# Kernel optimization log

Hardware: AMD Instinct MI355X
Metric: run time of the kernel (lower is better)

Reference implementation:

```python
import jax, jax.numpy as jnp
import numpy as np

B, S, D_MODEL, N_HEADS, MAX_LEN = 2, 1024, 1024, 16, 1024
D_K = D_MODEL // N_HEADS


def setup_inputs() -> dict:
    key = jax.random.key(0)
    ks = jax.random.split(key, 8)
    w_std = 1.0 / np.sqrt(D_MODEL)  # ~ torch Linear default scale
    inp = {
        "query": jax.random.normal(ks[0], (B, S, D_MODEL), jnp.float32),
        "key": jax.random.normal(ks[1], (B, S, D_MODEL), jnp.float32),
        "value": jax.random.normal(ks[2], (B, S, D_MODEL), jnp.float32),
        "Wq": jax.random.normal(ks[3], (D_MODEL, D_MODEL), jnp.float32) * w_std,
        "Wk": jax.random.normal(ks[4], (D_MODEL, D_MODEL), jnp.float32) * w_std,
        "Wv": jax.random.normal(ks[5], (D_MODEL, D_MODEL), jnp.float32) * w_std,
        "Wo": jax.random.normal(ks[6], (D_MODEL, D_MODEL), jnp.float32) * w_std,
        "bq": jnp.zeros((D_MODEL,), jnp.float32),
        "bk": jnp.zeros((D_MODEL,), jnp.float32),
        "bv": jnp.zeros((D_MODEL,), jnp.float32),
        "bo": jnp.zeros((D_MODEL,), jnp.float32),
        "Er": jax.random.normal(ks[7], (2 * MAX_LEN - 1, D_K), jnp.float32) * 0.02,
    }
    return inp


def _rel_positions(q_len, k_len, max_len):
    pos = jnp.arange(q_len)[:, None] - jnp.arange(k_len)[None, :]
    pos = jnp.clip(pos, -max_len + 1, max_len - 1)
    return pos + max_len - 1  # [q_len, k_len] indices into Er


def reference(query, key, value, Wq, Wk, Wv, Wo, bq, bk, bv, bo, Er):
    b, q_len, d_model = query.shape
    k_len = key.shape[1]
    d_k = Er.shape[-1]
    h = d_model // d_k
    scale = 1.0 / np.sqrt(d_k)

    def proj(x, W, bias):  # torch Linear: x @ W.T + b, then split heads -> [b,h,s,d_k]
        y = x @ W.T + bias
        return y.reshape(b, -1, h, d_k).transpose(0, 2, 1, 3)

    q = proj(query, Wq, bq)
    k = proj(key, Wk, bk)
    v = proj(value, Wv, bv)

    positions = _rel_positions(q_len, k_len, MAX_LEN)  # [q,k]
    # QEr[b,h,q,k] = sum_d q[b,h,q,d] * Er[positions[q,k], d]
    # computed as a full contraction against Er then a gather on the relative axis
    qe_all = jnp.einsum('bhqd,rd->bhqr', q, Er)  # [b,h,q,2*max_len-1]
    qer = jnp.take_along_axis(qe_all, positions[None, None, :, :], axis=-1)  # [b,h,q,k]

    qk = jnp.einsum('bhqd,bhkd->bhqk', q, k)
    scores = (qk + qer) * scale
    p_attn = jax.nn.softmax(scores, axis=-1)  # dropout=0.0 (eval)
    out = jnp.einsum('bhqk,bhkd->bhqd', p_attn, v)

    out = out.transpose(0, 2, 1, 3).reshape(b, q_len, h * d_k)
    return out @ Wo.T + bo
```

## Files before the change

kernel.cpp:

```cpp
#include <hip/hip_runtime.h>
#include <hip/hip_bf16.h>
#include <cstdint>
#include <cstddef>

typedef __attribute__((ext_vector_type(8))) short bf16x8;
typedef __attribute__((ext_vector_type(4))) float f32x4;
typedef unsigned short u16;
typedef unsigned int u32;

#define DEV static __device__ __forceinline__

constexpr int Sc = 1024, DMc = 1024, Hc = 16, DKc = 64;

DEV u16 f2bf(float f) {
  u32 u = __float_as_uint(f);
  return (u16)((u + 0x7FFFu + ((u >> 16) & 1u)) >> 16);
}
DEV float bf2f(u16 h) { return __uint_as_float(((u32)h) << 16); }

DEV void lds_fence() {
  asm volatile("s_waitcnt lgkmcnt(0)" ::: "memory");
  __builtin_amdgcn_sched_barrier(0);
}

#define GLDS16(g, l)                                                        \
  __builtin_amdgcn_global_load_lds(                                         \
      (const __attribute__((address_space(1))) void*)(g),                   \
      (__attribute__((address_space(3))) void*)(l), 16, 0, 0)

struct CvtJob { const float* in; u16* out; int nchunk; int rsh; };
struct CvtArgs { CvtJob j[8]; };

__global__ __launch_bounds__(256) void cvt_kernel(CvtArgs a) {
  CvtJob job = a.j[blockIdx.y];
  int ci = (int)(blockIdx.x * 256 + threadIdx.x);
  if (ci >= job.nchunk) return;
  const float* src = job.in + (size_t)ci * 8;
  float4 v0 = *(const float4*)src;
  float4 v1 = *(const float4*)(src + 4);
  bf16x8 o;
  o[0] = (short)f2bf(v0.x); o[1] = (short)f2bf(v0.y);
  o[2] = (short)f2bf(v0.z); o[3] = (short)f2bf(v0.w);
  o[4] = (short)f2bf(v1.x); o[5] = (short)f2bf(v1.y);
  o[6] = (short)f2bf(v1.z); o[7] = (short)f2bf(v1.w);
  int row = ci >> job.rsh;
  int co = (ci & ~7) | ((ci & 7) ^ (row & 7));
  *(bf16x8*)(job.out + (size_t)co * 8) = o;
}

struct GemmJob { const u16* A; const u16* W; const float* bias; void* out; };
struct GemmArgs { GemmJob p[3]; };

template<int BM, int MODE>
__global__ __launch_bounds__(256, 2) void gemm_bt(GemmArgs G) {
  constexpr int MI = BM / 32;
  __shared__ __align__(16) u16 sA[2][BM * 64];
  __shared__ __align__(16) u16 sB[2][128 * 64];
  const int tid = threadIdx.x, lane = tid & 63, w = tid >> 6;
  const int cl = lane & 15, rg = lane >> 4;
  const int srow = lane >> 3, schk = lane & 7;
  int z, m0, n0;
  if (MODE == 0) {
    int id = blockIdx.x;
    if (id < 256) { z = id >> 7; int r = id & 127; m0 = (r >> 3) * 128; n0 = (r & 7) * 128; }
    else          { z = 2;       int r = id - 256; m0 = (r >> 4) * 128; n0 = (r & 15) * 128; }
  } else {
    z = 0; int id = blockIdx.x; m0 = (id >> 3) * 64; n0 = (id & 7) * 128;
  }
  GemmJob P = G.p[z];
  constexpr int K = 1024;
  const int wm = (w >> 1) * (MI * 16), wn = (w & 1) * 64;
  f32x4 acc[MI][4] = {};

  auto stage = [&](int kt, int b) {
    const u16* Ab = P.A + (size_t)m0 * K + kt * 64;
    const u16* Wb = P.W + (size_t)n0 * K + kt * 64;
    #pragma unroll
    for (int i = 0; i < BM / 32; ++i)
      GLDS16(Ab + (size_t)(i * 32 + w * 8 + srow) * K + schk * 8, &sA[b][(i * 32 + w * 8) * 64]);
    #pragma unroll
    for (int i = 0; i < 4; ++i)
      GLDS16(Wb + (size_t)(i * 32 + w * 8 + srow) * K + schk * 8, &sB[b][(i * 32 + w * 8) * 64]);
  };

  stage(0, 0);
  for (int kt = 0; kt < 16; ++kt) {
    __syncthreads();
    if (kt < 15) stage(kt + 1, (kt + 1) & 1);
    const u16* A_ = sA[kt & 1];
    const u16* B_ = sB[kt & 1];
    #pragma unroll
    for (int kk = 0; kk < 2; ++kk) {
      bf16x8 af[MI], bfr[4];
      #pragma unroll
      for (int mi = 0; mi < MI; ++mi) {
        int row = wm + mi * 16 + cl;
        af[mi] = *(const bf16x8*)(A_ + row * 64 + ((kk * 4 + rg) ^ (row & 7)) * 8);
      }
      #pragma unroll
      for (int ni = 0; ni < 4; ++ni) {
        int row = wn + ni * 16 + cl;
        bfr[ni] = *(const bf16x8*)(B_ + row * 64 + ((kk * 4 + rg) ^ (row & 7)) * 8);
      }
      #pragma unroll
      for (int mi = 0; mi < MI; ++mi)
        #pragma unroll
        for (int ni = 0; ni < 4; ++ni)
          acc[mi][ni] = __builtin_amdgcn_mfma_f32_16x16x32_bf16(af[mi], bfr[ni], acc[mi][ni], 0, 0, 0);
    }
  }
  #pragma unroll
  for (int mi = 0; mi < MI; ++mi) {
    #pragma unroll
    for (int ni = 0; ni < 4; ++ni) {
      #pragma unroll
      for (int j = 0; j < 4; ++j) {
        int m = m0 + wm + mi * 16 + rg * 4 + j;
        int n = n0 + wn + ni * 16 + cl;
        if (MODE == 1) {
          ((float*)P.out)[(size_t)m * DMc + n] = acc[mi][ni][j] + P.bias[n];
        } else if (z < 2) {
          float v = acc[mi][ni][j] + P.bias[n];
          int h = n >> 6, d = n & 63;
          int c2 = (d >> 3) ^ (m & 7);
          ((u16*)P.out)[((size_t)((m >> 10) * Hc + h) * Sc + (m & 1023)) * DKc + c2 * 8 + (d & 7)] = f2bf(v);
        } else {
          float v = acc[mi][ni][j] + P.bias[m];
          int d = m & 63, h = m >> 6, bb = n >> 10, s = n & 1023;
          int c2 = ((s & 63) >> 3) ^ (d & 7);
          ((u16*)P.out)[((size_t)(bb * Hc + h) * DKc + d) * Sc + (s & ~63) + c2 * 8 + (s & 7)] = f2bf(v);
        }
      }
    }
  }
}

__global__ __launch_bounds__(256, 2) void attn_rel(
    const u16* __restrict__ qg, const u16* __restrict__ kg,
    const u16* __restrict__ vtg, const u16* __restrict__ erg,
    u16* __restrict__ og) {
  __shared__ __align__(16) u16 sK[2][64 * 64];
  __shared__ __align__(16) u16 sV[2][64 * 64];
  __shared__ __align__(16) u16 sT[4][16 * 80];
  __shared__ __align__(16) u16 sP[4][16 * 72];
  const int tid = threadIdx.x, lane = tid & 63, w = tid >> 6;
  const int cl = lane & 15, rg = lane >> 4;
  const int key = cl & 7;
  const int bh = blockIdx.x & 31, qt = blockIdx.x >> 5, q0 = qt * 64;

  const u16* qrow = qg + ((size_t)bh * Sc + q0 + w * 16 + cl) * DKc;
  bf16x8 qf0 = *(const bf16x8*)(qrow + (rg ^ key) * 8);
  bf16x8 qf1 = *(const bf16x8*)(qrow + ((rg + 4) ^ key) * 8);
  f32x4 oacc[4] = {};
  float lrow[4] = {0.f, 0.f, 0.f, 0.f};
  u16* Tw = sT[w];
  u16* Pw = sP[w];
  const u16* kbase = kg + (size_t)bh * Sc * DKc;
  const u16* vbase = vtg + (size_t)bh * DKc * Sc;

  auto stage = [&](int t, int b) {
    const u16* ks = kbase + t * 64 * 64;
    #pragma unroll
    for (int i = 0; i < 2; ++i) {
      GLDS16(ks + (i * 32 + w * 8) * 64 + lane * 8, &sK[b][(i * 32 + w * 8) * 64]);
      GLDS16(vbase + (size_t)(i * 32 + w * 8 + (lane >> 3)) * Sc + t * 64 + (lane & 7) * 8,
             &sV[b][(i * 32 + w * 8) * 64]);
    }
  };

  stage(0, 0);
  for (int t = 0; t < 16; ++t) {
    __syncthreads();
    if (t < 15) stage(t + 1, (t + 1) & 1);
    const u16* Kb = sK[t & 1];
    const u16* Vb = sV[t & 1];
    const u16* ebase = erg + (size_t)(q0 - t * 64 + 960) * DKc;

    f32x4 sc4[4];
    #pragma unroll
    for (int nc = 0; nc < 4; ++nc) {
      const u16* kr = Kb + (nc * 16 + cl) * 64;
      bf16x8 b0 = *(const bf16x8*)(kr + (rg ^ key) * 8);
      bf16x8 b1 = *(const bf16x8*)(kr + ((rg + 4) ^ key) * 8);
      f32x4 a = {};
      a = __builtin_amdgcn_mfma_f32_16x16x32_bf16(qf0, b0, a, 0, 0, 0);
      a = __builtin_amdgcn_mfma_f32_16x16x32_bf16(qf1, b1, a, 0, 0, 0);
      sc4[nc] = a;
    }
    #pragma unroll
    for (int rc0 = 0; rc0 < 5; ++rc0) {
      const u16* er = ebase + (size_t)((w + rc0) * 16 + cl) * DKc;
      bf16x8 b0 = *(const bf16x8*)(er + (rg ^ key) * 8);
      bf16x8 b1 = *(const bf16x8*)(er + ((rg + 4) ^ key) * 8);
      f32x4 a = {};
      a = __builtin_amdgcn_mfma_f32_16x16x32_bf16(qf0, b0, a, 0, 0, 0);
      a = __builtin_amdgcn_mfma_f32_16x16x32_bf16(qf1, b1, a, 0, 0, 0);
      #pragma unroll
      for (int j = 0; j < 4; ++j)
        Tw[(rg * 4 + j) * 80 + rc0 * 16 + cl] = f2bf(a[j]);
    }
    lds_fence();
    #pragma unroll
    for (int j = 0; j < 4; ++j) {
      const int qi = rg * 4 + j;
      #pragma unroll
      for (int nc = 0; nc < 4; ++nc) {
        int rl = qi + 63 - (nc * 16 + cl);
        float p = __expf((sc4[nc][j] + bf2f(Tw[qi * 80 + rl])) * 0.125f);
        lrow[j] += p;
        Pw[qi * 72 + nc * 16 + cl] = f2bf(p);
      }
    }
    lds_fence();
    bf16x8 pa0 = *(const bf16x8*)(Pw + cl * 72 + rg * 8);
    bf16x8 pa1 = *(const bf16x8*)(Pw + cl * 72 + 32 + rg * 8);
    #pragma unroll
    for (int dc = 0; dc < 4; ++dc) {
      const u16* vr = Vb + (dc * 16 + cl) * 64;
      bf16x8 b0 = *(const bf16x8*)(vr + (rg ^ key) * 8);
      bf16x8 b1 = *(const bf16x8*)(vr + ((rg + 4) ^ key) * 8);
      oacc[dc] = __builtin_amdgcn_mfma_f32_16x16x32_bf16(pa0, b0, oacc[dc], 0, 0, 0);
      oacc[dc] = __builtin_amdgcn_mfma_f32_16x16x32_bf16(pa1, b1, oacc[dc], 0, 0, 0);
    }
  }
  #pragma unroll
  for (int j = 0; j < 4; ++j) {
    float l = lrow[j];
    #pragma unroll
    for (int off = 1; off < 16; off <<= 1) l += __shfl_xor(l, off);
    lrow[j] = l;
  }
  const int b_ = bh >> 4, h = bh & 15;
  #pragma unroll
  for (int dc = 0; dc < 4; ++dc) {
    #pragma unroll
    for (int j = 0; j < 4; ++j) {
      int qr = q0 + w * 16 + rg * 4 + j;
      float v = oacc[dc][j] / lrow[j];
      int col = dc * 16 + cl;
      int c2 = (col >> 3) ^ (qr & 7);
      og[((size_t)(b_ * Sc + qr)) * DMc + h * 64 + c2 * 8 + (col & 7)] = f2bf(v);
    }
  }
}

extern "C" void kernel_launch(void* const* d_in, const int* in_sizes, int n_in,
                              void* d_out, int out_size, void* d_ws, size_t ws_size,
                              hipStream_t stream) {
  (void)in_sizes; (void)n_in; (void)out_size; (void)ws_size;
  const float* query = (const float*)d_in[0];
  const float* key_  = (const float*)d_in[1];
  const float* value = (const float*)d_in[2];
  const float* Wq = (const float*)d_in[3];
  const float* Wk = (const float*)d_in[4];
  const float* Wv = (const float*)d_in[5];
  const float* Wo = (const float*)d_in[6];
  const float* bq = (const float*)d_in[7];
  const float* bk = (const float*)d_in[8];
  const float* bv = (const float*)d_in[9];
  const float* bo = (const float*)d_in[10];
  const float* Er = (const float*)d_in[11];

  char* p = (char*)d_ws;
  size_t off = 0;
  auto alloc = [&](size_t bytes) {
    char* r = p + off;
    off += (bytes + 255) & ~(size_t)255;
    return r;
  };
  u16* Xq  = (u16*)alloc((size_t)2048 * 1024 * 2);
  u16* Xk  = (u16*)alloc((size_t)2048 * 1024 * 2);
  u16* Xv  = (u16*)alloc((size_t)2048 * 1024 * 2);
  u16* Wqb = (u16*)alloc((size_t)1024 * 1024 * 2);
  u16* Wkb = (u16*)alloc((size_t)1024 * 1024 * 2);
  u16* Wvb = (u16*)alloc((size_t)1024 * 1024 * 2);
  u16* Wob = (u16*)alloc((size_t)1024 * 1024 * 2);
  u16* Erb = (u16*)alloc((size_t)2048 * 64 * 2);
  u16* qh  = (u16*)alloc((size_t)2048 * 1024 * 2);
  u16* kh  = (u16*)alloc((size_t)2048 * 1024 * 2);
  u16* vt  = (u16*)alloc((size_t)2048 * 1024 * 2);
  u16* attnb = (u16*)alloc((size_t)2048 * 1024 * 2);

  CvtArgs ca;
  ca.j[0] = {query, Xq, 262144, 7};
  ca.j[1] = {key_,  Xk, 262144, 7};
  ca.j[2] = {value, Xv, 262144, 7};
  ca.j[3] = {Wq, Wqb, 131072, 7};
  ca.j[4] = {Wk, Wkb, 131072, 7};
  ca.j[5] = {Wv, Wvb, 131072, 7};
  ca.j[6] = {Wo, Wob, 131072, 7};
  ca.j[7] = {Er, Erb, 16376, 3};
  cvt_kernel<<<dim3(1024, 8, 1), 256, 0, stream>>>(ca);
  hipMemsetAsync(Erb + (size_t)2047 * 64, 0, 64 * sizeof(u16), stream);

  GemmArgs gp;
  gp.p[0] = {Xq, Wqb, bq, (void*)qh};
  gp.p[1] = {Xk, Wkb, bk, (void*)kh};
  gp.p[2] = {Wvb, Xv, bv, (void*)vt};
  gemm_bt<128, 0><<<dim3(384, 1, 1), 256, 0, stream>>>(gp);

  attn_rel<<<dim3(512, 1, 1), 256, 0, stream>>>(qh, kh, vt, Erb, attnb);

  GemmArgs go;
  go.p[0] = {attnb, Wob, bo, d_out};
  go.p[1] = go.p[0];
  go.p[2] = go.p[0];
  gemm_bt<64, 1><<<dim3(256, 1, 1), 256, 0, stream>>>(go);
}
```

Before: 106.2 us.

## Split attention over key halves with a merge kernel and pad LDS rows

Splits each attention block's 16 key tiles into two halves, so 1024 blocks are launched instead of 512, and writes unnormalized fp32 partial outputs and row sums to a workspace. A new merge kernel adds the two partials, normalizes them and writes the bf16 swizzled attention output. This is valid because the softmax uses no max subtraction. It also raises the occupancy hint to 3, pads the LDS row strides (80 to 84, 72 to 76) to reduce bank conflicts, and folds the Er padding memset into the convert kernel. The trade-off is extra fp32 traffic for the partials and one more kernel launch, in exchange for better CU fill on 256 CUs.

```diff
diff --git a/kernel.cpp b/kernel.cpp
--- a/kernel.cpp
+++ b/kernel.cpp
@@ -28,21 +28,23 @@
       (const __attribute__((address_space(1))) void*)(g),                   \
       (__attribute__((address_space(3))) void*)(l), 16, 0, 0)
 
-struct CvtJob { const float* in; u16* out; int nchunk; int rsh; };
+struct CvtJob { const float* in; u16* out; int nchunk; int rsh; int nreal; };
 struct CvtArgs { CvtJob j[8]; };
 
 __global__ __launch_bounds__(256) void cvt_kernel(CvtArgs a) {
   CvtJob job = a.j[blockIdx.y];
   int ci = (int)(blockIdx.x * 256 + threadIdx.x);
   if (ci >= job.nchunk) return;
-  const float* src = job.in + (size_t)ci * 8;
-  float4 v0 = *(const float4*)src;
-  float4 v1 = *(const float4*)(src + 4);
-  bf16x8 o;
-  o[0] = (short)f2bf(v0.x); o[1] = (short)f2bf(v0.y);
-  o[2] = (short)f2bf(v0.z); o[3] = (short)f2bf(v0.w);
-  o[4] = (short)f2bf(v1.x); o[5] = (short)f2bf(v1.y);
-  o[6] = (short)f2bf(v1.z); o[7] = (short)f2bf(v1.w);
+  bf16x8 o = {};
+  if (ci < job.nreal) {
+    const float* src = job.in + (size_t)ci * 8;
+    float4 v0 = *(const float4*)src;
+    float4 v1 = *(const float4*)(src + 4);
+    o[0] = (short)f2bf(v0.x); o[1] = (short)f2bf(v0.y);
+    o[2] = (short)f2bf(v0.z); o[3] = (short)f2bf(v0.w);
+    o[4] = (short)f2bf(v1.x); o[5] = (short)f2bf(v1.y);
+    o[6] = (short)f2bf(v1.z); o[7] = (short)f2bf(v1.w);
+  }
   int row = ci >> job.rsh;
   int co = (ci & ~7) | ((ci & 7) ^ (row & 7));
   *(bf16x8*)(job.out + (size_t)co * 8) = o;
@@ -135,18 +137,20 @@
   }
 }
 
-__global__ __launch_bounds__(256, 2) void attn_rel(
+__global__ __launch_bounds__(256, 3) void attn_rel(
     const u16* __restrict__ qg, const u16* __restrict__ kg,
     const u16* __restrict__ vtg, const u16* __restrict__ erg,
-    u16* __restrict__ og) {
+    float* __restrict__ Opart, float* __restrict__ lpart) {
   __shared__ __align__(16) u16 sK[2][64 * 64];
   __shared__ __align__(16) u16 sV[2][64 * 64];
-  __shared__ __align__(16) u16 sT[4][16 * 80];
-  __shared__ __align__(16) u16 sP[4][16 * 72];
+  __shared__ __align__(16) u16 sT[4][16 * 84];
+  __shared__ __align__(16) u16 sP[4][16 * 76];
   const int tid = threadIdx.x, lane = tid & 63, w = tid >> 6;
   const int cl = lane & 15, rg = lane >> 4;
   const int key = cl & 7;
-  const int bh = blockIdx.x & 31, qt = blockIdx.x >> 5, q0 = qt * 64;
+  const int bh = blockIdx.x & 31, qt = (blockIdx.x >> 5) & 15, half = blockIdx.x >> 9;
+  const int q0 = qt * 64;
+  const int t0 = half * 8;
 
   const u16* qrow = qg + ((size_t)bh * Sc + q0 + w * 16 + cl) * DKc;
   bf16x8 qf0 = *(const bf16x8*)(qrow + (rg ^ key) * 8);
@@ -168,12 +172,13 @@
     }
   };
 
-  stage(0, 0);
-  for (int t = 0; t < 16; ++t) {
+  stage(t0, 0);
+  for (int tt = 0; tt < 8; ++tt) {
+    const int t = t0 + tt;
     __syncthreads();
-    if (t < 15) stage(t + 1, (t + 1) & 1);
-    const u16* Kb = sK[t & 1];
-    const u16* Vb = sV[t & 1];
+    if (tt < 7) stage(t + 1, (tt + 1) & 1);
+    const u16* Kb = sK[tt & 1];
+    const u16* Vb = sV[tt & 1];
     const u16* ebase = erg + (size_t)(q0 - t * 64 + 960) * DKc;
 
     f32x4 sc4[4];
@@ -197,7 +202,7 @@
       a = __builtin_amdgcn_mfma_f32_16x16x32_bf16(qf1, b1, a, 0, 0, 0);
       #pragma unroll
       for (int j = 0; j < 4; ++j)
-        Tw[(rg * 4 + j) * 80 + rc0 * 16 + cl] = f2bf(a[j]);
+        Tw[(rg * 4 + j) * 84 + rc0 * 16 + cl] = f2bf(a[j]);
     }
     lds_fence();
     #pragma unroll
@@ -206,14 +211,14 @@
       #pragma unroll
       for (int nc = 0; nc < 4; ++nc) {
         int rl = qi + 63 - (nc * 16 + cl);
-        float p = __expf((sc4[nc][j] + bf2f(Tw[qi * 80 + rl])) * 0.125f);
+        float p = __expf((sc4[nc][j] + bf2f(Tw[qi * 84 + rl])) * 0.125f);
         lrow[j] += p;
-        Pw[qi * 72 + nc * 16 + cl] = f2bf(p);
+        Pw[qi * 76 + nc * 16 + cl] = f2bf(p);
       }
     }
     lds_fence();
-    bf16x8 pa0 = *(const bf16x8*)(Pw + cl * 72 + rg * 8);
-    bf16x8 pa1 = *(const bf16x8*)(Pw + cl * 72 + 32 + rg * 8);
+    bf16x8 pa0 = *(const bf16x8*)(Pw + cl * 76 + rg * 8);
+    bf16x8 pa1 = *(const bf16x8*)(Pw + cl * 76 + 32 + rg * 8);
     #pragma unroll
     for (int dc = 0; dc < 4; ++dc) {
       const u16* vr = Vb + (dc * 16 + cl) * 64;
@@ -230,18 +235,43 @@
     for (int off = 1; off < 16; off <<= 1) l += __shfl_xor(l, off);
     lrow[j] = l;
   }
-  const int b_ = bh >> 4, h = bh & 15;
+  float* Ob = Opart + (((size_t)(half * 32 + bh) * Sc + q0 + w * 16)) * DKc;
   #pragma unroll
-  for (int dc = 0; dc < 4; ++dc) {
-    #pragma unroll
-    for (int j = 0; j < 4; ++j) {
-      int qr = q0 + w * 16 + rg * 4 + j;
-      float v = oacc[dc][j] / lrow[j];
-      int col = dc * 16 + cl;
-      int c2 = (col >> 3) ^ (qr & 7);
-      og[((size_t)(b_ * Sc + qr)) * DMc + h * 64 + c2 * 8 + (col & 7)] = f2bf(v);
-    }
-  }
+  for (int dc = 0; dc < 4; ++dc)
+    #pragma unroll
+    for (int j = 0; j < 4; ++j)
+      Ob[(rg * 4 + j) * DKc + dc * 16 + cl] = oacc[dc][j];
+  if (cl == 0) {
+    #pragma unroll
+    for (int j = 0; j < 4; ++j)
+      lpart[(size_t)(half * 32 + bh) * Sc + q0 + w * 16 + rg * 4 + j] = lrow[j];
+  }
+}
+
+__global__ __launch_bounds__(256) void merge_kernel(
+    const float* __restrict__ O, const float* __restrict__ l,
+    u16* __restrict__ attnb) {
+  int ci = (int)(blockIdx.x * 256 + threadIdx.x);
+  int bh = ci >> 13, rem = ci & 8191, s = rem >> 3, dc = rem & 7;
+  const float* o0 = O + ((size_t)bh * Sc + s) * DKc + dc * 8;
+  const float* o1 = o0 + (size_t)32 * Sc * DKc;
+  float l0 = l[(size_t)bh * Sc + s];
+  float l1 = l[(size_t)(32 + bh) * Sc + s];
+  float rinv = 1.0f / (l0 + l1);
+  float4 a0 = ((const float4*)o0)[0], a1 = ((const float4*)o0)[1];
+  float4 b0 = ((const float4*)o1)[0], b1 = ((const float4*)o1)[1];
+  bf16x8 o;
+  o[0] = (short)f2bf((a0.x + b0.x) * rinv);
+  o[1] = (short)f2bf((a0.y + b0.y) * rinv);
+  o[2] = (short)f2bf((a0.z + b0.z) * rinv);
+  o[3] = (short)f2bf((a0.w + b0.w) * rinv);
+  o[4] = (short)f2bf((a1.x + b1.x) * rinv);
+  o[5] = (short)f2bf((a1.y + b1.y) * rinv);
+  o[6] = (short)f2bf((a1.z + b1.z) * rinv);
+  o[7] = (short)f2bf((a1.w + b1.w) * rinv);
+  int b = bh >> 4, h = bh & 15;
+  int c2 = dc ^ (s & 7);
+  *(bf16x8*)(attnb + ((size_t)(b * Sc + s)) * DMc + h * DKc + c2 * 8) = o;
 }
 
 extern "C" void kernel_launch(void* const* d_in, const int* in_sizes, int n_in,
@@ -280,18 +310,19 @@
   u16* kh  = (u16*)alloc((size_t)2048 * 1024 * 2);
   u16* vt  = (u16*)alloc((size_t)2048 * 1024 * 2);
   u16* attnb = (u16*)alloc((size_t)2048 * 1024 * 2);
+  float* Opart = (float*)alloc((size_t)2 * 32 * 1024 * 64 * 4);
+  float* lpart = (float*)alloc((size_t)2 * 32 * 1024 * 4);
 
   CvtArgs ca;
-  ca.j[0] = {query, Xq, 262144, 7};
-  ca.j[1] = {key_,  Xk, 262144, 7};
-  ca.j[2] = {value, Xv, 262144, 7};
-  ca.j[3] = {Wq, Wqb, 131072, 7};
-  ca.j[4] = {Wk, Wkb, 131072, 7};
-  ca.j[5] = {Wv, Wvb, 131072, 7};
-  ca.j[6] = {Wo, Wob, 131072, 7};
-  ca.j[7] = {Er, Erb, 16376, 3};
+  ca.j[0] = {query, Xq, 262144, 7, 262144};
+  ca.j[1] = {key_,  Xk, 262144, 7, 262144};
+  ca.j[2] = {value, Xv, 262144, 7, 262144};
+  ca.j[3] = {Wq, Wqb, 131072, 7, 131072};
+  ca.j[4] = {Wk, Wkb, 131072, 7, 131072};
+  ca.j[5] = {Wv, Wvb, 131072, 7, 131072};
+  ca.j[6] = {Wo, Wob, 131072, 7, 131072};
+  ca.j[7] = {Er, Erb, 16384, 3, 16376};
   cvt_kernel<<<dim3(1024, 8, 1), 256, 0, stream>>>(ca);
-  hipMemsetAsync(Erb + (size_t)2047 * 64, 0, 64 * sizeof(u16), stream);
 
   GemmArgs gp;
   gp.p[0] = {Xq, Wqb, bq, (void*)qh};
@@ -299,7 +330,9 @@
   gp.p[2] = {Wvb, Xv, bv, (void*)vt};
   gemm_bt<128, 0><<<dim3(384, 1, 1), 256, 0, stream>>>(gp);
 
-  attn_rel<<<dim3(512, 1, 1), 256, 0, stream>>>(qh, kh, vt, Erb, attnb);
+  attn_rel<<<dim3(1024, 1, 1), 256, 0, stream>>>(qh, kh, vt, Erb, Opart, lpart);
+
+  merge_kernel<<<dim3(1024, 1, 1), 256, 0, stream>>>(Opart, lpart, attnb);
 
   GemmArgs go;
   go.p[0] = {attnb, Wob, bo, d_out};
```

After: 113.8 us. +7.1%, slower.
